# Optimization experiments

Hardware: AMD Instinct MI355X
Metric: run time of the kernel (lower is better)

## Reference

```python
import jax, jax.numpy as jnp
import numpy as np
from jax import lax

B, T, D, K = 512, 512, 64, 1024
COMMITMENT_LOSS_FACTOR = 0.1
QUANTIZATION_LOSS_FACTOR = 0.2


def setup_inputs() -> dict:
    key = jax.random.key(0)
    k1, k2 = jax.random.split(key)
    h = jax.random.normal(k1, (B, T, D), dtype=jnp.float32)
    # codebook init: uniform(-1/K, 1/K), matching nn.Embedding init in the module
    weight = jax.random.uniform(k2, (K, D), dtype=jnp.float32, minval=-1.0 / K, maxval=1.0 / K)
    return {"h": h, "weight": weight}


def reference(h, weight):
    d = weight.shape[1]
    hf = h.reshape(-1, d)                                   # [N, D]
    # squared euclidean distances via expanded norms + matmul  -> [N, K]
    dist = ((hf ** 2).sum(-1, keepdims=True)
            + (weight ** 2).sum(-1)
            - 2.0 * hf @ weight.T)
    closest = jnp.argmin(dist, axis=-1)                     # [N]
    quantized_indices = closest[:, None]                    # [N, 1]
    # one_hot @ weight is exactly a row gather
    quantized = jnp.take(weight, closest, axis=0)           # [N, D]
    commitment_loss = ((lax.stop_gradient(quantized) - hf) ** 2).mean(-1)  # [N]
    embedding_loss = ((quantized - lax.stop_gradient(hf)) ** 2).mean(-1)   # [N]
    # straight-through estimator
    quantized_st = (hf + lax.stop_gradient(quantized - hf)).reshape(h.shape)
    loss = (commitment_loss * COMMITMENT_LOSS_FACTOR
            + embedding_loss * QUANTIZATION_LOSS_FACTOR)    # [N]
    return quantized_st, quantized_indices, loss
```

## Files before the change

### kernel.cpp

```cpp
#include <hip/hip_runtime.h>
#include <math.h>

#define NROWS (512 * 512)
#define KCB   1024
#define DDIM  64
#define NQ    ((size_t)NROWS * DDIM)
#define RPW   32
#define CMAX  8
#define WAVES 8
#define BLKT  512
#define KPH   512
#define NTPH  (KPH / 16)

typedef __attribute__((ext_vector_type(8))) short bf16x8;
typedef __attribute__((ext_vector_type(4))) float f32x4;

__device__ __forceinline__ unsigned short f2bf(float x) {
    unsigned u = __float_as_uint(x);
    u = u + 0x7FFFu + ((u >> 16) & 1u);
    return (unsigned short)(u >> 16);
}
__device__ __forceinline__ unsigned fsort(float d) {
    unsigned u = __float_as_uint(d);
    return (u & 0x80000000u) ? ~u : (u | 0x80000000u);
}

__global__ __launch_bounds__(1024)
void prep_w(const float* __restrict__ w, float* __restrict__ bsq,
            unsigned short* __restrict__ wbf, float* __restrict__ wmaxp) {
    __shared__ float red[16];
    const int k = threadIdx.x;
    const float* row = w + (size_t)k * DDIM;
    float r[8];
#pragma unroll
    for (int j = 0; j < 8; ++j) r[j] = __fmul_rn(row[j], row[j]);
#pragma unroll
    for (int i = 8; i < DDIM; i += 8)
#pragma unroll
        for (int j = 0; j < 8; ++j)
            r[j] = __fadd_rn(r[j], __fmul_rn(row[i + j], row[i + j]));
    float b = __fadd_rn(__fadd_rn(__fadd_rn(r[0], r[1]), __fadd_rn(r[2], r[3])),
                        __fadd_rn(__fadd_rn(r[4], r[5]), __fadd_rn(r[6], r[7])));
    bsq[k] = b;
    unsigned* dst = (unsigned*)(wbf + (size_t)k * DDIM);
#pragma unroll
    for (int j = 0; j < 32; ++j)
        dst[j] = (unsigned)f2bf(row[2 * j]) | ((unsigned)f2bf(row[2 * j + 1]) << 16);
    float v = sqrtf(b) * 1.02f;
#pragma unroll
    for (int off = 1; off < 64; off <<= 1) v = fmaxf(v, __shfl_xor(v, off));
    if ((threadIdx.x & 63) == 0) red[threadIdx.x >> 6] = v;
    __syncthreads();
    if (threadIdx.x == 0) {
        float m = red[0];
#pragma unroll
        for (int j = 1; j < 16; ++j) m = fmaxf(m, red[j]);
        *wmaxp = m;
    }
}

__global__ __launch_bounds__(BLKT, 4)
void vq_scan(const float* __restrict__ h, const float* __restrict__ w,
             const unsigned short* __restrict__ wbf, const float* __restrict__ bsq,
             const float* __restrict__ wmaxp, float* __restrict__ out) {
    __shared__ float4 s4[KPH * 8];
    __shared__ float sbsq[KPH];
    __shared__ int scnt[WAVES][RPW];
    __shared__ unsigned short sclist[WAVES][RPW][CMAX];
    __shared__ unsigned long long sbkey[WAVES][RPW];

    const int tid = threadIdx.x;
    const int wv = tid >> 6, lane = tid & 63;
    const int l16 = lane & 15, lh = lane >> 4;
    const int rowbase = blockIdx.x * (WAVES * RPW) + wv * RPW;

    if (lane < RPW) { scnt[wv][lane] = 0; sbkey[wv][lane] = 0xFFFFFFFFFFFFFFFFULL; }

    float af = 0.f;
    if (lane < RPW) {
        const float* row = h + (size_t)(rowbase + lane) * DDIM;
        float hr[DDIM];
#pragma unroll
        for (int i = 0; i < DDIM; i += 4) {
            float4 v = *reinterpret_cast<const float4*>(row + i);
            hr[i] = v.x; hr[i + 1] = v.y; hr[i + 2] = v.z; hr[i + 3] = v.w;
        }
        float s[8];
#pragma unroll
        for (int j = 0; j < 8; ++j) s[j] = __fmul_rn(hr[j], hr[j]);
#pragma unroll
        for (int i = 8; i < DDIM; i += 8)
#pragma unroll
            for (int j = 0; j < 8; ++j)
                s[j] = __fadd_rn(s[j], __fmul_rn(hr[i + j], hr[i + j]));
        af = __fadd_rn(__fadd_rn(__fadd_rn(s[0], s[1]), __fadd_rn(s[2], s[3])),
                       __fadd_rn(__fadd_rn(s[4], s[5]), __fadd_rn(s[6], s[7])));
    }

    bf16x8 afr[2][2];
#pragma unroll
    for (int mt = 0; mt < 2; ++mt) {
        const float* hrow = h + ((size_t)(rowbase + mt * 16 + l16)) * DDIM;
#pragma unroll
        for (int dh = 0; dh < 2; ++dh) {
            float4 a = *reinterpret_cast<const float4*>(hrow + dh * 32 + lh * 8);
            float4 bq = *reinterpret_cast<const float4*>(hrow + dh * 32 + lh * 8 + 4);
            union { bf16x8 v; unsigned short u[8]; } pk;
            pk.u[0] = f2bf(a.x); pk.u[1] = f2bf(a.y); pk.u[2] = f2bf(a.z); pk.u[3] = f2bf(a.w);
            pk.u[4] = f2bf(bq.x); pk.u[5] = f2bf(bq.y); pk.u[6] = f2bf(bq.z); pk.u[7] = f2bf(bq.w);
            afr[mt][dh] = pk.v;
        }
    }

    const int sw = l16 & 7;
    const int C0 = lh ^ sw;
    const int C1 = (4 + lh) ^ sw;

    float pmin[8];
#pragma unroll
    for (int j = 0; j < 8; ++j) pmin[j] = INFINITY;

    const float4* g4all = reinterpret_cast<const float4*>(wbf);

#pragma unroll 1
    for (int ph = 0; ph < 2; ++ph) {
        const int k0 = ph * KPH;
        __syncthreads();
        const float4* g4 = g4all + (size_t)k0 * 8;
#pragma unroll
        for (int j = 0; j < 8; ++j) {
            int F = j * BLKT + tid;
            int r = F >> 3, c = F & 7;
            s4[F] = g4[r * 8 + (c ^ (r & 7))];
        }
        sbsq[tid] = bsq[k0 + tid];
        __syncthreads();

        float4 pb0[2], pb1[2];
        float pbq[2];
#pragma unroll
        for (int q = 0; q < 2; ++q) {
            const int lr = q * 16 + l16;
            pb0[q] = s4[lr * 8 + C0];
            pb1[q] = s4[lr * 8 + C1];
            pbq[q] = sbsq[lr];
        }
#pragma unroll 4
        for (int nt = 0; nt < NTPH; ++nt) {
            const int s = nt & 1;
            float4 b0 = pb0[s], b1 = pb1[s];
            float bq = pbq[s];
            {
                const int ntn = (nt + 2 < NTPH) ? (nt + 2) : (NTPH - 1);
                const int lr = ntn * 16 + l16;
                pb0[s] = s4[lr * 8 + C0];
                pb1[s] = s4[lr * 8 + C1];
                pbq[s] = sbsq[lr];
            }
            bf16x8 bfr0 = *reinterpret_cast<const bf16x8*>(&b0);
            bf16x8 bfr1 = *reinterpret_cast<const bf16x8*>(&b1);
#pragma unroll
            for (int mt = 0; mt < 2; ++mt) {
                f32x4 acc = {0.f, 0.f, 0.f, 0.f};
                acc = __builtin_amdgcn_mfma_f32_16x16x32_bf16(afr[mt][0], bfr0, acc, 0, 0, 0);
                acc = __builtin_amdgcn_mfma_f32_16x16x32_bf16(afr[mt][1], bfr1, acc, 0, 0, 0);
#pragma unroll
                for (int i = 0; i < 4; ++i)
                    pmin[mt * 4 + i] = fminf(pmin[mt * 4 + i], bq - (acc[i] + acc[i]));
            }
        }
    }

#pragma unroll
    for (int off = 1; off < 16; off <<= 1)
#pragma unroll
        for (int j = 0; j < 8; ++j) pmin[j] = fminf(pmin[j], __shfl_xor(pmin[j], off));
    const float wmaxv = *wmaxp;
    float tr[8];
#pragma unroll
    for (int mt = 0; mt < 2; ++mt)
#pragma unroll
        for (int i = 0; i < 4; ++i) {
            float Afr = __shfl(af, mt * 16 + lh * 4 + i);
            tr[mt * 4 + i] = pmin[mt * 4 + i] + sqrtf(Afr) * 1.001f * wmaxv * 0.03125f + 1e-3f;
        }

#pragma unroll 1
    for (int ph = 0; ph < 2; ++ph) {
        const int k0 = ph * KPH;
        __syncthreads();
        const float4* g4 = g4all + (size_t)k0 * 8;
#pragma unroll
        for (int j = 0; j < 8; ++j) {
            int F = j * BLKT + tid;
            int r = F >> 3, c = F & 7;
            s4[F] = g4[r * 8 + (c ^ (r & 7))];
        }
        sbsq[tid] = bsq[k0 + tid];
        __syncthreads();

        float4 pb0[2], pb1[2];
        float pbq[2];
#pragma unroll
        for (int q = 0; q < 2; ++q) {
            const int lr = q * 16 + l16;
            pb0[q] = s4[lr * 8 + C0];
            pb1[q] = s4[lr * 8 + C1];
            pbq[q] = sbsq[lr];
        }
#pragma unroll 4
        for (int nt = 0; nt < NTPH; ++nt) {
            const int s = nt & 1;
            float4 b0 = pb0[s], b1 = pb1[s];
            float bq = pbq[s];
            {
                const int ntn = (nt + 2 < NTPH) ? (nt + 2) : (NTPH - 1);
                const int lr = ntn * 16 + l16;
                pb0[s] = s4[lr * 8 + C0];
                pb1[s] = s4[lr * 8 + C1];
                pbq[s] = sbsq[lr];
            }
            bf16x8 bfr0 = *reinterpret_cast<const bf16x8*>(&b0);
            bf16x8 bfr1 = *reinterpret_cast<const bf16x8*>(&b1);
            const int kk = k0 + nt * 16 + l16;
#pragma unroll
            for (int mt = 0; mt < 2; ++mt) {
                f32x4 acc = {0.f, 0.f, 0.f, 0.f};
                acc = __builtin_amdgcn_mfma_f32_16x16x32_bf16(afr[mt][0], bfr0, acc, 0, 0, 0);
                acc = __builtin_amdgcn_mfma_f32_16x16x32_bf16(afr[mt][1], bfr1, acc, 0, 0, 0);
#pragma unroll
                for (int i = 0; i < 4; ++i) {
                    float val = bq - (acc[i] + acc[i]);
                    if (val <= tr[mt * 4 + i]) {
                        int row = mt * 16 + lh * 4 + i;
                        int slot = atomicAdd(&scnt[wv][row], 1);
                        if (slot < CMAX) sclist[wv][row][slot] = (unsigned short)kk;
                    }
                }
            }
        }
    }
    __builtin_amdgcn_wave_barrier();

    {
        const int row = lane >> 1;
        const int s0 = lane & 1;
        const float Afr = __shfl(af, row);
        const int cnt = scnt[wv][row];
        if (cnt <= CMAX && s0 < cnt) {
            const size_t ng = (size_t)rowbase + row;
            const float* hrow = h + ng * DDIM;
            float hreg[DDIM];
#pragma unroll
            for (int i = 0; i < DDIM; i += 4) {
                float4 v = *reinterpret_cast<const float4*>(hrow + i);
                hreg[i] = v.x; hreg[i + 1] = v.y; hreg[i + 2] = v.z; hreg[i + 3] = v.w;
            }
            for (int slot = s0; slot < cnt; slot += 2) {
                int k = sclist[wv][row][slot];
                const float* wr = w + (size_t)k * DDIM;
                float acc = 0.f;
#pragma unroll
                for (int i = 0; i < DDIM; i += 4) {
                    float4 x = *reinterpret_cast<const float4*>(wr + i);
                    acc = fmaf(hreg[i + 0], x.x, acc);
                    acc = fmaf(hreg[i + 1], x.y, acc);
                    acc = fmaf(hreg[i + 2], x.z, acc);
                    acc = fmaf(hreg[i + 3], x.w, acc);
                }
                float d = __fsub_rn(__fadd_rn(Afr, bsq[k]), __fadd_rn(acc, acc));
                unsigned long long key = ((unsigned long long)fsort(d) << 32) | (unsigned)k;
                atomicMin(&sbkey[wv][row], key);
            }
        }
    }
#pragma unroll 1
    for (int r = 0; r < RPW; ++r) {
        const float Afr = __shfl(af, r);
        if (scnt[wv][r] > CMAX) {
            const size_t ng = (size_t)rowbase + r;
            const float* hrow = h + ng * DDIM;
            float hreg[DDIM];
#pragma unroll
            for (int i = 0; i < DDIM; i += 4) {
                float4 v = *reinterpret_cast<const float4*>(hrow + i);
                hreg[i] = v.x; hreg[i + 1] = v.y; hreg[i + 2] = v.z; hreg[i + 3] = v.w;
            }
            for (int k = lane; k < KCB; k += 64) {
                const float* wr = w + (size_t)k * DDIM;
                float acc = 0.f;
#pragma unroll
                for (int i = 0; i < DDIM; i += 4) {
                    float4 x = *reinterpret_cast<const float4*>(wr + i);
                    acc = fmaf(hreg[i + 0], x.x, acc);
                    acc = fmaf(hreg[i + 1], x.y, acc);
                    acc = fmaf(hreg[i + 2], x.z, acc);
                    acc = fmaf(hreg[i + 3], x.w, acc);
                }
                float d = __fsub_rn(__fadd_rn(Afr, bsq[k]), __fadd_rn(acc, acc));
                unsigned long long key = ((unsigned long long)fsort(d) << 32) | (unsigned)k;
                atomicMin(&sbkey[wv][r], key);
            }
        }
    }
    __builtin_amdgcn_wave_barrier();

    if (lane < RPW)
        out[NQ + rowbase + lane] = (float)(unsigned)(sbkey[wv][lane] & 0xFFFFFFFFu);

#pragma unroll
    for (int q = 0; q < 8; ++q) {
        const int idx = q * 64 + lane;
        const int row = idx >> 4, c4 = idx & 15;
        const int bk = (int)(unsigned)(sbkey[wv][row] & 0xFFFFFFFFu);
        const size_t ng = (size_t)rowbase + row;
        float4 hq = *reinterpret_cast<const float4*>(h + ng * DDIM + 4 * c4);
        float4 wq = *reinterpret_cast<const float4*>(w + (size_t)bk * DDIM + 4 * c4);
        float4 o;
        o.x = __fadd_rn(hq.x, __fsub_rn(wq.x, hq.x));
        o.y = __fadd_rn(hq.y, __fsub_rn(wq.y, hq.y));
        o.z = __fadd_rn(hq.z, __fsub_rn(wq.z, hq.z));
        o.w = __fadd_rn(hq.w, __fsub_rn(wq.w, hq.w));
        *reinterpret_cast<float4*>(out + ng * DDIM + 4 * c4) = o;
    }

    if (lane < RPW) {
        const int bk = (int)(unsigned)(sbkey[wv][lane] & 0xFFFFFFFFu);
        const size_t ng = (size_t)rowbase + lane;
        const float* hrow = h + ng * DDIM;
        const float* qrow = w + (size_t)bk * DDIM;
        float hr[DDIM];
#pragma unroll
        for (int i = 0; i < DDIM; i += 4) {
            float4 v = *reinterpret_cast<const float4*>(hrow + i);
            hr[i] = v.x; hr[i + 1] = v.y; hr[i + 2] = v.z; hr[i + 3] = v.w;
        }
        float r2[8];
#pragma unroll
        for (int c = 0; c < 8; ++c) {
            float4 qa = *reinterpret_cast<const float4*>(qrow + 8 * c);
            float4 qb = *reinterpret_cast<const float4*>(qrow + 8 * c + 4);
            float d0 = __fsub_rn(qa.x, hr[8 * c + 0]);
            float d1 = __fsub_rn(qa.y, hr[8 * c + 1]);
            float d2 = __fsub_rn(qa.z, hr[8 * c + 2]);
            float d3 = __fsub_rn(qa.w, hr[8 * c + 3]);
            float d4 = __fsub_rn(qb.x, hr[8 * c + 4]);
            float d5 = __fsub_rn(qb.y, hr[8 * c + 5]);
            float d6 = __fsub_rn(qb.z, hr[8 * c + 6]);
            float d7 = __fsub_rn(qb.w, hr[8 * c + 7]);
            if (c == 0) {
                r2[0] = __fmul_rn(d0, d0); r2[1] = __fmul_rn(d1, d1);
                r2[2] = __fmul_rn(d2, d2); r2[3] = __fmul_rn(d3, d3);
                r2[4] = __fmul_rn(d4, d4); r2[5] = __fmul_rn(d5, d5);
                r2[6] = __fmul_rn(d6, d6); r2[7] = __fmul_rn(d7, d7);
            } else {
                r2[0] = __fadd_rn(r2[0], __fmul_rn(d0, d0));
                r2[1] = __fadd_rn(r2[1], __fmul_rn(d1, d1));
                r2[2] = __fadd_rn(r2[2], __fmul_rn(d2, d2));
                r2[3] = __fadd_rn(r2[3], __fmul_rn(d3, d3));
                r2[4] = __fadd_rn(r2[4], __fmul_rn(d4, d4));
                r2[5] = __fadd_rn(r2[5], __fmul_rn(d5, d5));
                r2[6] = __fadd_rn(r2[6], __fmul_rn(d6, d6));
                r2[7] = __fadd_rn(r2[7], __fmul_rn(d7, d7));
            }
        }
        float S = __fadd_rn(__fadd_rn(__fadd_rn(r2[0], r2[1]), __fadd_rn(r2[2], r2[3])),
                            __fadd_rn(__fadd_rn(r2[4], r2[5]), __fadd_rn(r2[6], r2[7])));
        float m = __fmul_rn(S, 0.015625f);
        out[NQ + NROWS + ng] = __fadd_rn(__fmul_rn(m, 0.1f), __fmul_rn(m, 0.2f));
    }
}

extern "C" void kernel_launch(void* const* d_in, const int* in_sizes, int n_in,
                              void* d_out, int out_size, void* d_ws, size_t ws_size,
                              hipStream_t stream) {
    (void)in_sizes; (void)n_in; (void)out_size; (void)ws_size;
    const float* h = (const float*)d_in[0];
    const float* w = (const float*)d_in[1];
    float* out = (float*)d_out;

    char* ws = (char*)d_ws;
    float* bsq = (float*)ws;
    float* wmaxp = (float*)(ws + 4096);
    unsigned short* wbf = (unsigned short*)(ws + 8192);

    prep_w<<<1, 1024, 0, stream>>>(w, bsq, wbf, wmaxp);
    vq_scan<<<NROWS / (WAVES * RPW), BLKT, 0, stream>>>(h, w, wbf, bsq, wmaxp, out);
}
```

Baseline: 286.1 us.

## Replace two-pass codebook scan with single pass keeping per-lane top-3 packed keys

The second full MFMA pass over the codebook, which gathered candidates under a threshold, is removed. During the single scan each lane now keeps its three smallest distances, with the codebook index packed into the low mantissa bits. After the scan the threshold is computed and candidates are taken from these per-lane lists. A flag forces the exact full-scan fallback for a row whenever a lane's third-best key falls inside the threshold, since that lane may have dropped further candidates. The codebook tile per phase is halved, and the top-3 bookkeeping adds several min/max ops per element.

Result: slower. 339.3 us (+18.6%).

```diff
diff --git a/kernel.cpp b/kernel.cpp
--- a/kernel.cpp
+++ b/kernel.cpp
@@ -9,7 +9,7 @@
 #define CMAX  8
 #define WAVES 8
 #define BLKT  512
-#define KPH   512
+#define KPH   256
 #define NTPH  (KPH / 16)
 
 typedef __attribute__((ext_vector_type(8))) short bf16x8;
@@ -68,13 +68,18 @@
     __shared__ int scnt[WAVES][RPW];
     __shared__ unsigned short sclist[WAVES][RPW][CMAX];
     __shared__ unsigned long long sbkey[WAVES][RPW];
+    __shared__ int sflag[WAVES][RPW];
 
     const int tid = threadIdx.x;
     const int wv = tid >> 6, lane = tid & 63;
     const int l16 = lane & 15, lh = lane >> 4;
     const int rowbase = blockIdx.x * (WAVES * RPW) + wv * RPW;
 
-    if (lane < RPW) { scnt[wv][lane] = 0; sbkey[wv][lane] = 0xFFFFFFFFFFFFFFFFULL; }
+    if (lane < RPW) {
+        scnt[wv][lane] = 0;
+        sflag[wv][lane] = 0;
+        sbkey[wv][lane] = 0xFFFFFFFFFFFFFFFFULL;
+    }
 
     float af = 0.f;
     if (lane < RPW) {
@@ -116,24 +121,24 @@
     const int C0 = lh ^ sw;
     const int C1 = (4 + lh) ^ sw;
 
-    float pmin[8];
-#pragma unroll
-    for (int j = 0; j < 8; ++j) pmin[j] = INFINITY;
+    float key1[8], key2[8], key3[8];
+#pragma unroll
+    for (int j = 0; j < 8; ++j) { key1[j] = INFINITY; key2[j] = INFINITY; key3[j] = INFINITY; }
 
     const float4* g4all = reinterpret_cast<const float4*>(wbf);
 
 #pragma unroll 1
-    for (int ph = 0; ph < 2; ++ph) {
+    for (int ph = 0; ph < 4; ++ph) {
         const int k0 = ph * KPH;
         __syncthreads();
         const float4* g4 = g4all + (size_t)k0 * 8;
 #pragma unroll
-        for (int j = 0; j < 8; ++j) {
+        for (int j = 0; j < 4; ++j) {
             int F = j * BLKT + tid;
             int r = F >> 3, c = F & 7;
             s4[F] = g4[r * 8 + (c ^ (r & 7))];
         }
-        sbsq[tid] = bsq[k0 + tid];
+        if (tid < KPH) sbsq[tid] = bsq[k0 + tid];
         __syncthreads();
 
         float4 pb0[2], pb1[2];
@@ -159,22 +164,36 @@
             }
             bf16x8 bfr0 = *reinterpret_cast<const bf16x8*>(&b0);
             bf16x8 bfr1 = *reinterpret_cast<const bf16x8*>(&b1);
+            const unsigned kk = (unsigned)(k0 + nt * 16 + l16);
 #pragma unroll
             for (int mt = 0; mt < 2; ++mt) {
                 f32x4 acc = {0.f, 0.f, 0.f, 0.f};
                 acc = __builtin_amdgcn_mfma_f32_16x16x32_bf16(afr[mt][0], bfr0, acc, 0, 0, 0);
                 acc = __builtin_amdgcn_mfma_f32_16x16x32_bf16(afr[mt][1], bfr1, acc, 0, 0, 0);
 #pragma unroll
-                for (int i = 0; i < 4; ++i)
-                    pmin[mt * 4 + i] = fminf(pmin[mt * 4 + i], bq - (acc[i] + acc[i]));
-            }
-        }
-    }
-
+                for (int i = 0; i < 4; ++i) {
+                    const int j = mt * 4 + i;
+                    float val = bq - (acc[i] + acc[i]);
+                    float key = __uint_as_float((__float_as_uint(val) & 0xFFFFFC00u) | kk);
+                    float m1 = fminf(key1[j], key);
+                    float M1 = fmaxf(key1[j], key);
+                    float m2 = fminf(key2[j], M1);
+                    float M2 = fmaxf(key2[j], M1);
+                    float m3 = fminf(key3[j], M2);
+                    key1[j] = m1; key2[j] = m2; key3[j] = m3;
+                }
+            }
+        }
+    }
+
+    float gmin[8];
+#pragma unroll
+    for (int j = 0; j < 8; ++j) gmin[j] = key1[j];
 #pragma unroll
     for (int off = 1; off < 16; off <<= 1)
 #pragma unroll
-        for (int j = 0; j < 8; ++j) pmin[j] = fminf(pmin[j], __shfl_xor(pmin[j], off));
+        for (int j = 0; j < 8; ++j) gmin[j] = fminf(gmin[j], __shfl_xor(gmin[j], off));
+
     const float wmaxv = *wmaxp;
     float tr[8];
 #pragma unroll
@@ -182,62 +201,24 @@
 #pragma unroll
         for (int i = 0; i < 4; ++i) {
             float Afr = __shfl(af, mt * 16 + lh * 4 + i);
-            tr[mt * 4 + i] = pmin[mt * 4 + i] + sqrtf(Afr) * 1.001f * wmaxv * 0.03125f + 1e-3f;
-        }
-
-#pragma unroll 1
-    for (int ph = 0; ph < 2; ++ph) {
-        const int k0 = ph * KPH;
-        __syncthreads();
-        const float4* g4 = g4all + (size_t)k0 * 8;
-#pragma unroll
-        for (int j = 0; j < 8; ++j) {
-            int F = j * BLKT + tid;
-            int r = F >> 3, c = F & 7;
-            s4[F] = g4[r * 8 + (c ^ (r & 7))];
-        }
-        sbsq[tid] = bsq[k0 + tid];
-        __syncthreads();
-
-        float4 pb0[2], pb1[2];
-        float pbq[2];
-#pragma unroll
-        for (int q = 0; q < 2; ++q) {
-            const int lr = q * 16 + l16;
-            pb0[q] = s4[lr * 8 + C0];
-            pb1[q] = s4[lr * 8 + C1];
-            pbq[q] = sbsq[lr];
-        }
-#pragma unroll 4
-        for (int nt = 0; nt < NTPH; ++nt) {
-            const int s = nt & 1;
-            float4 b0 = pb0[s], b1 = pb1[s];
-            float bq = pbq[s];
-            {
-                const int ntn = (nt + 2 < NTPH) ? (nt + 2) : (NTPH - 1);
-                const int lr = ntn * 16 + l16;
-                pb0[s] = s4[lr * 8 + C0];
-                pb1[s] = s4[lr * 8 + C1];
-                pbq[s] = sbsq[lr];
-            }
-            bf16x8 bfr0 = *reinterpret_cast<const bf16x8*>(&b0);
-            bf16x8 bfr1 = *reinterpret_cast<const bf16x8*>(&b1);
-            const int kk = k0 + nt * 16 + l16;
-#pragma unroll
-            for (int mt = 0; mt < 2; ++mt) {
-                f32x4 acc = {0.f, 0.f, 0.f, 0.f};
-                acc = __builtin_amdgcn_mfma_f32_16x16x32_bf16(afr[mt][0], bfr0, acc, 0, 0, 0);
-                acc = __builtin_amdgcn_mfma_f32_16x16x32_bf16(afr[mt][1], bfr1, acc, 0, 0, 0);
-#pragma unroll
-                for (int i = 0; i < 4; ++i) {
-                    float val = bq - (acc[i] + acc[i]);
-                    if (val <= tr[mt * 4 + i]) {
-                        int row = mt * 16 + lh * 4 + i;
-                        int slot = atomicAdd(&scnt[wv][row], 1);
-                        if (slot < CMAX) sclist[wv][row][slot] = (unsigned short)kk;
-                    }
-                }
-            }
+            tr[mt * 4 + i] = gmin[mt * 4 + i] + sqrtf(Afr) * 1.001f * wmaxv * 0.03125f + 1e-3f;
+        }
+
+#pragma unroll
+    for (int j = 0; j < 8; ++j) {
+        const int row = (j >> 2) * 16 + lh * 4 + (j & 3);
+        if (key1[j] <= tr[j]) {
+            int slot = atomicAdd(&scnt[wv][row], 1);
+            if (slot < CMAX) sclist[wv][row][slot] = (unsigned short)(__float_as_uint(key1[j]) & 1023u);
+        }
+        if (key2[j] <= tr[j]) {
+            int slot = atomicAdd(&scnt[wv][row], 1);
+            if (slot < CMAX) sclist[wv][row][slot] = (unsigned short)(__float_as_uint(key2[j]) & 1023u);
+        }
+        if (key3[j] <= tr[j]) {
+            int slot = atomicAdd(&scnt[wv][row], 1);
+            if (slot < CMAX) sclist[wv][row][slot] = (unsigned short)(__float_as_uint(key3[j]) & 1023u);
+            sflag[wv][row] = 1;
         }
     }
     __builtin_amdgcn_wave_barrier();
@@ -277,7 +258,7 @@
 #pragma unroll 1
     for (int r = 0; r < RPW; ++r) {
         const float Afr = __shfl(af, r);
-        if (scnt[wv][r] > CMAX) {
+        if (scnt[wv][r] > CMAX || sflag[wv][r]) {
             const size_t ng = (size_t)rowbase + r;
             const float* hrow = h + ng * DDIM;
             float hreg[DDIM];
```
